# Kernel optimization log

Measured on AMD Instinct MI355X. Metric: run time of the kernel, lower is better.

Reference implementation:

```python
import jax, jax.numpy as jnp
import numpy as np


def setup_inputs() -> dict:
    key = jax.random.key(0)
    k0, k1, k2, k3, k4 = jax.random.split(key, 5)
    B, N, H, d, kproj = 4, 2048, 8, 32, 256
    queries = jax.random.normal(k0, (B, N, H, d), dtype=jnp.float32)
    keys = jax.random.normal(k1, (B, N, H, d), dtype=jnp.float32)
    values = jax.random.normal(k2, (B, N, H, d), dtype=jnp.float32)
    # Linformer sequence projections [N, k]; scaled so projected K/V keep unit-ish variance
    E_proj = jax.random.normal(k3, (N, kproj), dtype=jnp.float32) * 0.02
    F_proj = jax.random.normal(k4, (N, kproj), dtype=jnp.float32) * 0.02
    return {"queries": queries, "keys": keys, "values": values,
            "E_proj": E_proj, "F_proj": F_proj}


def reference(queries, keys, values, E_proj, F_proj):
    """Hybrid attention of dsfa_former:
      (1) FullAttention with triangular causal mask (manual einsum+softmax)
      (2) LinearAttentionHead: Linformer-style sequence projection of K/V via E/F.
    Dropout is identity (eval). Returns (out_full, out_lin), each [B, N, H, d].
    """
    B, N, H, d = queries.shape
    scale = 1.0 / jnp.sqrt(jnp.asarray(d, queries.dtype))

    # ---- FullAttention (causal) ----
    scores = jnp.einsum('blhe,bshe->bhls', queries, keys)  # [B,H,N,N]
    causal = jnp.triu(jnp.ones((N, N), dtype=bool), k=1)   # True above diag -> masked
    scores = jnp.where(causal, -jnp.inf, scores)
    A = jax.nn.softmax(scale * scores, axis=-1)
    out_full = jnp.einsum('bhls,bshd->blhd', A, values)    # [B,N,H,d]

    # ---- LinearAttentionHead (Linformer, no causal mask since kp != N) ----
    Qb = queries.transpose(0, 2, 1, 3)  # [B,H,N,d]
    Kb = keys.transpose(0, 2, 1, 3)
    Vb = values.transpose(0, 2, 1, 3)
    Kp = jnp.einsum('bhnd,nk->bhkd', Kb, E_proj)           # [B,H,k,d]
    Vp = jnp.einsum('bhnd,nk->bhkd', Vb, F_proj)           # [B,H,k,d]
    s_lin = jnp.einsum('bhnd,bhkd->bhnk', Qb, Kp) * scale  # d_k == d
    P = jax.nn.softmax(s_lin, axis=-1)
    out_lin = jnp.einsum('bhnk,bhkd->bhnd', P, Vp).transpose(0, 2, 1, 3)  # [B,N,H,d]

    return out_full, out_lin
```

## Files before the change

### kernel.cpp

```cpp
#include <hip/hip_runtime.h>
#include <hip/hip_bf16.h>


typedef __bf16 bf16x8 __attribute__((ext_vector_type(8)));
typedef __bf16 bf16x2 __attribute__((ext_vector_type(2)));
typedef float f32x4 __attribute__((ext_vector_type(4)));

union BF8 { uint4 u4; ushort us[8]; bf16x8 b; unsigned u32[4]; };

constexpr int B_ = 4, N_ = 2048, H_ = 8, D_ = 32, KP_ = 256, BH_ = 32;
constexpr float SCL2 = 0.25505654442633533f;
constexpr int NFULL = 1024;
constexpr int CHK = 32 * D_;

__device__ __forceinline__ ushort f2bf(float f) {
  unsigned u = __builtin_bit_cast(unsigned, f);
  return (ushort)((u + 0x7FFFu + ((u >> 16) & 1u)) >> 16);
}
__device__ __forceinline__ unsigned pkbf(float f0, float f1) {
#if __has_builtin(__builtin_amdgcn_cvt_pk_bf16_f32)
  bf16x2 r = __builtin_amdgcn_cvt_pk_bf16_f32(f0, f1);
  return __builtin_bit_cast(unsigned, r);
#else
  unsigned u0 = __builtin_bit_cast(unsigned, f0) + 0x8000u;
  unsigned u1 = __builtin_bit_cast(unsigned, f1) + 0x8000u;
  return __builtin_amdgcn_perm(u1, u0, 0x07060302);
#endif
}
__device__ __forceinline__ float bflo(unsigned u) {
  return __builtin_bit_cast(float, u << 16);
}
__device__ __forceinline__ float bfhi(unsigned u) {
  return __builtin_bit_cast(float, u & 0xFFFF0000u);
}
__device__ __forceinline__ float ex2(float x) {
#if __has_builtin(__builtin_amdgcn_exp2f)
  return __builtin_amdgcn_exp2f(x);
#else
  return exp2f(x);
#endif
}

__device__ __forceinline__ void load8_bf(const float* __restrict__ p,
                                         float scale, BF8& hi) {
  float4 a = *reinterpret_cast<const float4*>(p);
  float4 b = *reinterpret_cast<const float4*>(p + 4);
  float x[8] = {a.x, a.y, a.z, a.w, b.x, b.y, b.z, b.w};
#pragma unroll
  for (int i = 0; i < 8; ++i) hi.us[i] = f2bf(x[i] * scale);
}

__global__ __launch_bounds__(256) void k_prep(const float* __restrict__ K,
                                              const float* __restrict__ V,
                                              const float* __restrict__ E,
                                              const float* __restrict__ F,
                                              ushort* __restrict__ KH,
                                              ushort* __restrict__ Kt,
                                              ushort* __restrict__ Vt,
                                              ushort* __restrict__ Et,
                                              ushort* __restrict__ Ft) {
  __shared__ alignas(16) ushort S[4224];
  const int idx = blockIdx.x;
  const int t = threadIdx.x;
  if (idx < 1024) {
    ushort* Tk = S;
    ushort* Tv = S + 2112;
    const int bh = idx >> 5, b = bh >> 3, h = bh & 7;
    const int n0 = (idx & 31) * 64;
    {
      const int row = t >> 2, e8 = (t & 3) * 8;
      const size_t gbase = ((size_t)(b * N_ + n0 + row) * H_ + h) * D_ + e8;
      float4 k0 = *reinterpret_cast<const float4*>(K + gbase);
      float4 k1 = *reinterpret_cast<const float4*>(K + gbase + 4);
      float4 v0 = *reinterpret_cast<const float4*>(V + gbase);
      float4 v1 = *reinterpret_cast<const float4*>(V + gbase + 4);
      float kk[8] = {k0.x,k0.y,k0.z,k0.w,k1.x,k1.y,k1.z,k1.w};
      float vv[8] = {v0.x,v0.y,v0.z,v0.w,v1.x,v1.y,v1.z,v1.w};
      BF8 xh, vh;
#pragma unroll
      for (int i = 0; i < 4; ++i) {
        xh.u32[i] = pkbf(kk[2 * i], kk[2 * i + 1]);
        vh.u32[i] = pkbf(vv[2 * i], vv[2 * i + 1]);
      }
#pragma unroll
      for (int i = 0; i < 8; ++i) {
        Tk[(e8 + i) * 66 + row] = xh.us[i];
        Tv[(e8 + i) * 66 + row] = vh.us[i];
      }
      *reinterpret_cast<uint4*>(KH + ((size_t)bh * N_ + n0 + row) * D_ + e8) = xh.u4;
    }
    __syncthreads();
    {
      const int e = t >> 3, n8 = (t & 7) * 8;
      BF8 xk, xv;
#pragma unroll
      for (int i = 0; i < 8; ++i) {
        xk.us[i] = Tk[e * 66 + n8 + i];
        xv.us[i] = Tv[e * 66 + n8 + i];
      }
      const int c = (n0 + n8) >> 5, k = n8 & 31;
      const size_t ob = (((size_t)bh * 64 + c) * 32 + e) * 32 + k;
      *reinterpret_cast<uint4*>(Kt + ob) = xk.u4;
      *reinterpret_cast<uint4*>(Vt + ob) = xv.u4;
    }
  } else {
    const int j = idx - 1024;
    const float* src = (j >> 7) ? F : E;
    ushort* dst = (j >> 7) ? Ft : Et;
    const int jj = j & 127;
    const int n0 = (jj & 31) * 64, kp0 = (jj >> 5) * 64;
    ushort* T = S;
    {
      const int n = t >> 2, c16 = (t & 3) * 16;
      const size_t gbase = (size_t)(n0 + n) * KP_ + kp0 + c16;
#pragma unroll
      for (int q = 0; q < 4; ++q) {
        float4 x = *reinterpret_cast<const float4*>(src + gbase + q * 4);
        const unsigned u01 = pkbf(x.x, x.y), u23 = pkbf(x.z, x.w);
        T[(c16 + q * 4 + 0) * 66 + n] = (ushort)u01;
        T[(c16 + q * 4 + 1) * 66 + n] = (ushort)(u01 >> 16);
        T[(c16 + q * 4 + 2) * 66 + n] = (ushort)u23;
        T[(c16 + q * 4 + 3) * 66 + n] = (ushort)(u23 >> 16);
      }
    }
    __syncthreads();
    {
      const int kp = t >> 2, n16 = (t & 3) * 16;
      BF8 x0, x1;
#pragma unroll
      for (int i = 0; i < 8; ++i) {
        x0.us[i] = T[kp * 66 + n16 + i];
        x1.us[i] = T[kp * 66 + n16 + 8 + i];
      }
      const int c = (n0 + n16) >> 5, k = n16 & 31;
      const size_t ob = ((size_t)c * KP_ + kp0 + kp) * 32 + k;
      *reinterpret_cast<uint4*>(dst + ob) = x0.u4;
      *reinterpret_cast<uint4*>(dst + ob + 8) = x1.u4;
    }
  }
}

__global__ __launch_bounds__(512) void k_linproj(const ushort* __restrict__ Et,
                                                 const ushort* __restrict__ Ft,
                                                 const ushort* __restrict__ Kt,
                                                 const ushort* __restrict__ Vt,
                                                 ushort* __restrict__ Kp,
                                                 ushort* __restrict__ Vpt) {
  __shared__ float L[8][64][16];
  const int id = blockIdx.x;
  const int bh = (id & 7) + 8 * ((id >> 3) & 3);
  const int kp16 = (id >> 5) * 16;
  const int t = threadIdx.x;
  const int w = t >> 6, lane = t & 63, quad = lane >> 4, l15 = lane & 15;
  const int cbase = w * 8;

  const ushort* eA = Et + ((size_t)cbase * KP_ + kp16 + l15) * 32 + quad * 8;
  const ushort* fA = Ft + ((size_t)cbase * KP_ + kp16 + l15) * 32 + quad * 8;
  const ushort* kB0 = Kt + (((size_t)bh * 64 + cbase) * 32 + l15) * 32 + quad * 8;
  const ushort* kB1 = kB0 + 512;
  const ushort* vB0 = Vt + (((size_t)bh * 64 + cbase) * 32 + l15) * 32 + quad * 8;
  const ushort* vB1 = vB0 + 512;

  f32x4 accK0 = {0.f,0.f,0.f,0.f}, accK1 = {0.f,0.f,0.f,0.f};
  f32x4 accV0 = {0.f,0.f,0.f,0.f}, accV1 = {0.f,0.f,0.f,0.f};

  BF8 e0, f0, k00, k10, v00, v10;
  BF8 e1, f1, k01, k11, v01, v11;

#define LPLD(E, F, K0, K1, V0, V1, I)                                   \
  do {                                                                  \
    (E).u4 = *reinterpret_cast<const uint4*>(eA + (size_t)(I) * (KP_ * 32)); \
    (F).u4 = *reinterpret_cast<const uint4*>(fA + (size_t)(I) * (KP_ * 32)); \
    (K0).u4 = *reinterpret_cast<const uint4*>(kB0 + (I) * CHK);         \
    (K1).u4 = *reinterpret_cast<const uint4*>(kB1 + (I) * CHK);         \
    (V0).u4 = *reinterpret_cast<const uint4*>(vB0 + (I) * CHK);         \
    (V1).u4 = *reinterpret_cast<const uint4*>(vB1 + (I) * CHK);         \
  } while (0)
#define LPMM(E, F, K0, K1, V0, V1)                                            \
  do {                                                                        \
    accK0 = __builtin_amdgcn_mfma_f32_16x16x32_bf16((E).b, (K0).b, accK0, 0, 0, 0); \
    accK1 = __builtin_amdgcn_mfma_f32_16x16x32_bf16((E).b, (K1).b, accK1, 0, 0, 0); \
    accV0 = __builtin_amdgcn_mfma_f32_16x16x32_bf16((F).b, (V0).b, accV0, 0, 0, 0); \
    accV1 = __builtin_amdgcn_mfma_f32_16x16x32_bf16((F).b, (V1).b, accV1, 0, 0, 0); \
  } while (0)

  LPLD(e0, f0, k00, k10, v00, v10, 0);
  LPLD(e1, f1, k01, k11, v01, v11, 1);
#pragma unroll
  for (int p = 0; p < 3; ++p) {
    LPMM(e0, f0, k00, k10, v00, v10);
    LPLD(e0, f0, k00, k10, v00, v10, 2 * p + 2);
    LPMM(e1, f1, k01, k11, v01, v11);
    LPLD(e1, f1, k01, k11, v01, v11, 2 * p + 3);
  }
  LPMM(e0, f0, k00, k10, v00, v10);
  LPMM(e1, f1, k01, k11, v01, v11);
#undef LPLD
#undef LPMM

#pragma unroll
  for (int r = 0; r < 4; ++r) {
    L[w][lane][r]      = accK0[r];
    L[w][lane][4 + r]  = accK1[r];
    L[w][lane][8 + r]  = accV0[r];
    L[w][lane][12 + r] = accV1[r];
  }
  __syncthreads();
  if (w < 4) {
#pragma unroll
    for (int r = 0; r < 4; ++r) {
      const float v = ((L[0][lane][w * 4 + r] + L[1][lane][w * 4 + r]) +
                       (L[2][lane][w * 4 + r] + L[3][lane][w * 4 + r])) +
                      ((L[4][lane][w * 4 + r] + L[5][lane][w * 4 + r]) +
                       (L[6][lane][w * 4 + r] + L[7][lane][w * 4 + r]));
      const int kp = kp16 + quad * 4 + r;
      if (w == 0)      Kp[((size_t)bh * KP_ + kp) * D_ + l15]       = f2bf(v);
      else if (w == 1) Kp[((size_t)bh * KP_ + kp) * D_ + 16 + l15]  = f2bf(v);
      else if (w == 2)
        Vpt[(((size_t)bh * 8 + (kp >> 5)) * 32 + l15) * 32 + (kp & 31)] = f2bf(v);
      else
        Vpt[(((size_t)bh * 8 + (kp >> 5)) * 32 + 16 + l15) * 32 + (kp & 31)] = f2bf(v);
    }
  }
}

__global__ __launch_bounds__(256, 4) void k_attn(const float* __restrict__ Q,
                                                 const ushort* __restrict__ KH,
                                                 const ushort* __restrict__ Vt,
                                                 const ushort* __restrict__ Kp,
                                                 const ushort* __restrict__ Vpt,
                                                 float* __restrict__ out) {
  __shared__ alignas(16) unsigned Op[4][4][64][4];
  __shared__ float Ls[4][4][4][4];
  const int idx = blockIdx.x;
  const int t = threadIdx.x;
  const int w = t >> 6, lane = t & 63;
  const int quad = lane >> 4, l15 = lane & 15;
  const int kperm1 = 8 * (l15 >> 2) + (l15 & 3);
  const f32x4 z = {0.f,0.f,0.f,0.f};

  BF8 ones;
#pragma unroll
  for (int i2 = 0; i2 < 4; ++i2) ones.u32[i2] = 0x3F803F80u;

  const int bh = (idx & 7) + 8 * ((idx >> 3) & 3);
  const int m = 31 - (idx >> 5);
  const int b = bh >> 3, h = bh & 7;
  const int q0 = 64 * m;

  BF8 qh[4];
#pragma unroll
  for (int tt = 0; tt < 4; ++tt)
    load8_bf(Q + ((size_t)(b * N_ + q0 + 16 * tt + l15) * H_ + h) * D_ + quad * 8,
             SCL2, qh[tt]);

  {
    const ushort* KHl = KH + (size_t)bh * N_ * D_ + (size_t)kperm1 * D_ + quad * 8;
    const ushort* V0l = Vt + (size_t)bh * N_ * D_ + l15 * 32 + quad * 8;
    const ushort* V1l = V0l + 512;

    const int nun = 2 * m;
    const int cb = (w * nun) >> 2;
    const int ce = ((w + 1) * nun) >> 2;
    const int nwu = ce - cb;

    f32x4 O0[4], O1[4], LS[4];
#pragma unroll
    for (int tt = 0; tt < 4; ++tt) { O0[tt] = z; O1[tt] = z; LS[tt] = z; }

    BF8 kA1, kA2, vA0, vA1, kB1, kB2, vB0, vB1;

    auto procU = [&](BF8& k1, BF8& k2, BF8& v0, BF8& v1) {
      __builtin_amdgcn_s_setprio(1);
#pragma unroll
      for (int tt = 0; tt < 4; ++tt) {
        f32x4 s1 = __builtin_amdgcn_mfma_f32_16x16x32_bf16(k1.b, qh[tt].b, z, 0, 0, 0);
        f32x4 s2 = __builtin_amdgcn_mfma_f32_16x16x32_bf16(k2.b, qh[tt].b, z, 0, 0, 0);
        float e0 = ex2(s1[0]), e1 = ex2(s1[1]), e2 = ex2(s1[2]), e3 = ex2(s1[3]);
        float e4 = ex2(s2[0]), e5 = ex2(s2[1]), e6 = ex2(s2[2]), e7 = ex2(s2[3]);
        BF8 p;
        p.u32[0] = pkbf(e0, e1); p.u32[1] = pkbf(e2, e3);
        p.u32[2] = pkbf(e4, e5); p.u32[3] = pkbf(e6, e7);
        O0[tt] = __builtin_amdgcn_mfma_f32_16x16x32_bf16(p.b, v0.b, O0[tt], 0, 0, 0);
        O1[tt] = __builtin_amdgcn_mfma_f32_16x16x32_bf16(p.b, v1.b, O1[tt], 0, 0, 0);
        LS[tt] = __builtin_amdgcn_mfma_f32_16x16x32_bf16(p.b, ones.b, LS[tt], 0, 0, 0);
      }
      __builtin_amdgcn_s_setprio(0);
    };
    auto procM = [&](BF8& k1, BF8& k2, BF8& v0, BF8& v1, int ta, bool doUnm) {
      __builtin_amdgcn_s_setprio(1);
#pragma unroll
      for (int d = 0; d < 2; ++d) {
        const int tt = ta + d;
        const int thr = d ? 16 + l15 : l15;
        f32x4 s1 = __builtin_amdgcn_mfma_f32_16x16x32_bf16(k1.b, qh[tt].b, z, 0, 0, 0);
        f32x4 s2 = __builtin_amdgcn_mfma_f32_16x16x32_bf16(k2.b, qh[tt].b, z, 0, 0, 0);
        float e[8];
#pragma unroll
        for (int j = 0; j < 8; ++j) {
          const float sv = (j < 4) ? s1[j] : s2[j - 4];
          e[j] = (8 * quad + j <= thr) ? ex2(sv) : 0.f;
        }
        BF8 p;
        p.u32[0] = pkbf(e[0], e[1]); p.u32[1] = pkbf(e[2], e[3]);
        p.u32[2] = pkbf(e[4], e[5]); p.u32[3] = pkbf(e[6], e[7]);
        O0[tt] = __builtin_amdgcn_mfma_f32_16x16x32_bf16(p.b, v0.b, O0[tt], 0, 0, 0);
        O1[tt] = __builtin_amdgcn_mfma_f32_16x16x32_bf16(p.b, v1.b, O1[tt], 0, 0, 0);
        LS[tt] = __builtin_amdgcn_mfma_f32_16x16x32_bf16(p.b, ones.b, LS[tt], 0, 0, 0);
      }
      if (doUnm) {
#pragma unroll
        for (int tt = 2; tt < 4; ++tt) {
          f32x4 s1 = __builtin_amdgcn_mfma_f32_16x16x32_bf16(k1.b, qh[tt].b, z, 0, 0, 0);
          f32x4 s2 = __builtin_amdgcn_mfma_f32_16x16x32_bf16(k2.b, qh[tt].b, z, 0, 0, 0);
          float e0 = ex2(s1[0]), e1 = ex2(s1[1]), e2 = ex2(s1[2]), e3 = ex2(s1[3]);
          float e4 = ex2(s2[0]), e5 = ex2(s2[1]), e6 = ex2(s2[2]), e7 = ex2(s2[3]);
          BF8 p;
          p.u32[0] = pkbf(e0, e1); p.u32[1] = pkbf(e2, e3);
          p.u32[2] = pkbf(e4, e5); p.u32[3] = pkbf(e6, e7);
          O0[tt] = __builtin_amdgcn_mfma_f32_16x16x32_bf16(p.b, v0.b, O0[tt], 0, 0, 0);
          O1[tt] = __builtin_amdgcn_mfma_f32_16x16x32_bf16(p.b, v1.b, O1[tt], 0, 0, 0);
          LS[tt] = __builtin_amdgcn_mfma_f32_16x16x32_bf16(p.b, ones.b, LS[tt], 0, 0, 0);
        }
      }
      __builtin_amdgcn_s_setprio(0);
    };

    kA1.u4 = *reinterpret_cast<const uint4*>(KHl + (size_t)cb * CHK);
    kA2.u4 = *reinterpret_cast<const uint4*>(KHl + (size_t)cb * CHK + 4 * D_);
    vA0.u4 = *reinterpret_cast<const uint4*>(V0l + (size_t)cb * CHK);
    vA1.u4 = *reinterpret_cast<const uint4*>(V1l + (size_t)cb * CHK);
    kB1.u4 = *reinterpret_cast<const uint4*>(KHl + (size_t)(cb + 1) * CHK);
    kB2.u4 = *reinterpret_cast<const uint4*>(KHl + (size_t)(cb + 1) * CHK + 4 * D_);
    vB0.u4 = *reinterpret_cast<const uint4*>(V0l + (size_t)(cb + 1) * CHK);
    vB1.u4 = *reinterpret_cast<const uint4*>(V1l + (size_t)(cb + 1) * CHK);

    const ushort* pKA = KHl + (size_t)(cb + 2) * CHK;
    const ushort* pKB = KHl + (size_t)(cb + 3) * CHK;
    const ushort* pV0 = V0l + (size_t)(cb + 2) * CHK;
    const ushort* pV1 = V1l + (size_t)(cb + 2) * CHK;

    int i = 0;
    for (; i + 2 <= nwu; i += 2) {
      procU(kA1, kA2, vA0, vA1);
      kA1.u4 = *reinterpret_cast<const uint4*>(pKA);
      kA2.u4 = *reinterpret_cast<const uint4*>(pKA + 4 * D_);
      vA0.u4 = *reinterpret_cast<const uint4*>(pV0);
      vA1.u4 = *reinterpret_cast<const uint4*>(pV1);
      procU(kB1, kB2, vB0, vB1);
      kB1.u4 = *reinterpret_cast<const uint4*>(pKB);
      kB2.u4 = *reinterpret_cast<const uint4*>(pKB + 4 * D_);
      vB0.u4 = *reinterpret_cast<const uint4*>(pV0 + CHK);
      vB1.u4 = *reinterpret_cast<const uint4*>(pV1 + CHK);
      pKA += 2 * CHK; pKB += 2 * CHK; pV0 += 2 * CHK; pV1 += 2 * CHK;
    }
    if (i < nwu) {
      procU(kA1, kA2, vA0, vA1);
      if (w == 3) procM(kB1, kB2, vB0, vB1, 0, true);
    } else if (w == 3) {
      procM(kA1, kA2, vA0, vA1, 0, true);
    }
    if (w == 2) {
      const int c2 = nun + 1;
      kB1.u4 = *reinterpret_cast<const uint4*>(KHl + (size_t)c2 * CHK);
      kB2.u4 = *reinterpret_cast<const uint4*>(KHl + (size_t)c2 * CHK + 4 * D_);
      vB0.u4 = *reinterpret_cast<const uint4*>(V0l + (size_t)c2 * CHK);
      vB1.u4 = *reinterpret_cast<const uint4*>(V1l + (size_t)c2 * CHK);
      procM(kB1, kB2, vB0, vB1, 2, false);
    }

#pragma unroll
    for (int tt = 0; tt < 4; ++tt) {
      uint4 pk;
      pk.x = pkbf(O0[tt][0], O0[tt][1]);
      pk.y = pkbf(O0[tt][2], O0[tt][3]);
      pk.z = pkbf(O1[tt][0], O1[tt][1]);
      pk.w = pkbf(O1[tt][2], O1[tt][3]);
      *reinterpret_cast<uint4*>(Op[w][tt][lane]) = pk;
    }
    if (l15 == 0) {
#pragma unroll
      for (int tt = 0; tt < 4; ++tt)
#pragma unroll
        for (int r = 0; r < 4; ++r) Ls[w][tt][quad][r] = LS[tt][r];
    }
    __syncthreads();
    {
      const int tt = w;
      float iv[4];
#pragma unroll
      for (int r = 0; r < 4; ++r) {
        const float l = Ls[0][tt][quad][r] + Ls[1][tt][quad][r] +
                        Ls[2][tt][quad][r] + Ls[3][tt][quad][r];
        iv[r] = __builtin_amdgcn_rcpf(l);
      }
      float A0[4] = {0.f,0.f,0.f,0.f}, A1[4] = {0.f,0.f,0.f,0.f};
#pragma unroll
      for (int s = 0; s < 4; ++s) {
        const uint4 u = *reinterpret_cast<const uint4*>(Op[s][tt][lane]);
        A0[0] += bflo(u.x); A0[1] += bfhi(u.x);
        A0[2] += bflo(u.y); A0[3] += bfhi(u.y);
        A1[0] += bflo(u.z); A1[1] += bfhi(u.z);
        A1[2] += bflo(u.w); A1[3] += bfhi(u.w);
      }
#pragma unroll
      for (int r = 0; r < 4; ++r) {
        const int q = q0 + 16 * tt + quad * 4 + r;
        const size_t base = ((size_t)(b * N_ + q) * H_ + h) * D_;
        out[base + l15]      = A0[r] * iv[r];
        out[base + 16 + l15] = A1[r] * iv[r];
      }
    }
  }

  {
    BF8 qsel = qh[0];
    if (w == 1) qsel = qh[1];
    else if (w == 2) qsel = qh[2];
    else if (w == 3) qsel = qh[3];

    float* olin = out + (size_t)B_ * N_ * H_ * D_;
    const int q0l = q0 + 16 * w;

    const int kperm2 = kperm1 + 4;
    const ushort* KpHb = Kp + (size_t)bh * KP_ * D_ + quad * 8;
    const ushort* Vp0 = Vpt + (size_t)bh * KP_ * D_ + l15 * 32 + quad * 8;
    const ushort* Vp1 = Vp0 + 512;

    f32x4 LSum = z, O0 = z, O1 = z;
    __builtin_amdgcn_s_setprio(1);
#pragma unroll
    for (int g = 0; g < 8; ++g) {
      const int kp0 = g * 32;
      BF8 a1, a2, v0, v1;
      a1.u4 = *reinterpret_cast<const uint4*>(KpHb + (size_t)(kp0 + kperm1) * D_);
      a2.u4 = *reinterpret_cast<const uint4*>(KpHb + (size_t)(kp0 + kperm2) * D_);
      v0.u4 = *reinterpret_cast<const uint4*>(Vp0 + g * CHK);
      v1.u4 = *reinterpret_cast<const uint4*>(Vp1 + g * CHK);
      f32x4 s1 = __builtin_amdgcn_mfma_f32_16x16x32_bf16(a1.b, qsel.b, z, 0, 0, 0);
      f32x4 s2 = __builtin_amdgcn_mfma_f32_16x16x32_bf16(a2.b, qsel.b, z, 0, 0, 0);
      const float e0 = ex2(s1[0]), e1 = ex2(s1[1]), e2 = ex2(s1[2]), e3 = ex2(s1[3]);
      const float e4 = ex2(s2[0]), e5 = ex2(s2[1]), e6 = ex2(s2[2]), e7 = ex2(s2[3]);
      BF8 p;
      p.u32[0] = pkbf(e0, e1); p.u32[1] = pkbf(e2, e3);
      p.u32[2] = pkbf(e4, e5); p.u32[3] = pkbf(e6, e7);
      LSum = __builtin_amdgcn_mfma_f32_16x16x32_bf16(p.b, ones.b, LSum, 0, 0, 0);
      O0 = __builtin_amdgcn_mfma_f32_16x16x32_bf16(p.b, v0.b, O0, 0, 0, 0);
      O1 = __builtin_amdgcn_mfma_f32_16x16x32_bf16(p.b, v1.b, O1, 0, 0, 0);
    }
    __builtin_amdgcn_s_setprio(0);

#pragma unroll
    for (int r = 0; r < 4; ++r) {
      const float fr = __builtin_amdgcn_rcpf(LSum[r]);
      const int q = q0l + quad * 4 + r;
      const size_t base = ((size_t)(b * N_ + q) * H_ + h) * D_;
      olin[base + l15]      = O0[r] * fr;
      olin[base + 16 + l15] = O1[r] * fr;
    }
  }
}

extern "C" void kernel_launch(void* const* d_in, const int* in_sizes, int n_in,
                              void* d_out, int out_size, void* d_ws, size_t ws_size,
                              hipStream_t stream) {
  const float* Q = (const float*)d_in[0];
  const float* K = (const float*)d_in[1];
  const float* V = (const float*)d_in[2];
  const float* E = (const float*)d_in[3];
  const float* F = (const float*)d_in[4];
  float* out = (float*)d_out;

  ushort* KH  = (ushort*)d_ws;
  ushort* Kt  = KH + (size_t)BH_ * N_ * D_;
  ushort* Vt  = Kt + (size_t)BH_ * N_ * D_;
  ushort* Et  = Vt + (size_t)BH_ * N_ * D_;
  ushort* Ft  = Et + (size_t)KP_ * N_;
  ushort* Kp  = Ft + (size_t)KP_ * N_;
  ushort* Vpt = Kp + (size_t)BH_ * KP_ * D_;

  k_prep<<<dim3(1280), 256, 0, stream>>>(K, V, E, F, KH, Kt, Vt, Et, Ft);
  k_linproj<<<dim3(512), 512, 0, stream>>>(Et, Ft, Kt, Vt, Kp, Vpt);
  k_attn<<<dim3(NFULL), 256, 0, stream>>>(Q, KH, Vt, Kp, Vpt, out);
}
```

Baseline: 122.6 us.

## Pre-convert Q to bf16 in prep and store K/Kp in MFMA-fragment layout

Q is now scaled and converted to bf16 in the prep kernel and written in a per-tile fragment layout, so the attention kernel loads ready-made bf16 operands instead of fp32 with per-element conversion. KH and Kp are likewise stored in a lane-permuted chunk layout, so each lane's MFMA operand is a contiguous 16-byte read at laneoff instead of a strided row gather. This cuts global traffic and conversion work in k_attn at the cost of an extra bf16 Q write and more workspace in the prep stage.

```diff
diff --git a/kernel.cpp b/kernel.cpp
--- a/kernel.cpp
+++ b/kernel.cpp
@@ -41,16 +41,8 @@
 #endif
 }
 
-__device__ __forceinline__ void load8_bf(const float* __restrict__ p,
-                                         float scale, BF8& hi) {
-  float4 a = *reinterpret_cast<const float4*>(p);
-  float4 b = *reinterpret_cast<const float4*>(p + 4);
-  float x[8] = {a.x, a.y, a.z, a.w, b.x, b.y, b.z, b.w};
-#pragma unroll
-  for (int i = 0; i < 8; ++i) hi.us[i] = f2bf(x[i] * scale);
-}
-
-__global__ __launch_bounds__(256) void k_prep(const float* __restrict__ K,
+__global__ __launch_bounds__(256) void k_prep(const float* __restrict__ Qf,
+                                              const float* __restrict__ K,
                                               const float* __restrict__ V,
                                               const float* __restrict__ E,
                                               const float* __restrict__ F,
@@ -58,7 +50,8 @@
                                               ushort* __restrict__ Kt,
                                               ushort* __restrict__ Vt,
                                               ushort* __restrict__ Et,
-                                              ushort* __restrict__ Ft) {
+                                              ushort* __restrict__ Ft,
+                                              ushort* __restrict__ QH) {
   __shared__ alignas(16) ushort S[4224];
   const int idx = blockIdx.x;
   const int t = threadIdx.x;
@@ -74,20 +67,37 @@
       float4 k1 = *reinterpret_cast<const float4*>(K + gbase + 4);
       float4 v0 = *reinterpret_cast<const float4*>(V + gbase);
       float4 v1 = *reinterpret_cast<const float4*>(V + gbase + 4);
+      float4 q0 = *reinterpret_cast<const float4*>(Qf + gbase);
+      float4 q1 = *reinterpret_cast<const float4*>(Qf + gbase + 4);
       float kk[8] = {k0.x,k0.y,k0.z,k0.w,k1.x,k1.y,k1.z,k1.w};
       float vv[8] = {v0.x,v0.y,v0.z,v0.w,v1.x,v1.y,v1.z,v1.w};
-      BF8 xh, vh;
+      float qq[8] = {q0.x,q0.y,q0.z,q0.w,q1.x,q1.y,q1.z,q1.w};
+      BF8 xh, vh, qp;
 #pragma unroll
       for (int i = 0; i < 4; ++i) {
         xh.u32[i] = pkbf(kk[2 * i], kk[2 * i + 1]);
         vh.u32[i] = pkbf(vv[2 * i], vv[2 * i + 1]);
+        qp.u32[i] = pkbf(qq[2 * i] * SCL2, qq[2 * i + 1] * SCL2);
       }
 #pragma unroll
       for (int i = 0; i < 8; ++i) {
         Tk[(e8 + i) * 66 + row] = xh.us[i];
         Tv[(e8 + i) * 66 + row] = vh.us[i];
       }
-      *reinterpret_cast<uint4*>(KH + ((size_t)bh * N_ + n0 + row) * D_ + e8) = xh.u4;
+      {
+        const int n32 = row & 31;
+        const int cg = (idx & 31) * 2 + (row >> 5);
+        const int half = (n32 >> 2) & 1;
+        const int l15p = 4 * (n32 >> 3) + (n32 & 3);
+        *reinterpret_cast<uint4*>(
+            KH + (((size_t)bh * 64 + cg) * 2 + half) * 512 + l15p * 32 + e8) = xh.u4;
+      }
+      {
+        const int mq = idx & 31;
+        const int tq = (row >> 4) & 3, l15q = row & 15;
+        *reinterpret_cast<uint4*>(
+            QH + (((size_t)bh * 32 + mq) * 4 + tq) * 512 + l15q * 32 + e8) = qp.u4;
+      }
     }
     __syncthreads();
     {
@@ -214,17 +224,22 @@
                       ((L[4][lane][w * 4 + r] + L[5][lane][w * 4 + r]) +
                        (L[6][lane][w * 4 + r] + L[7][lane][w * 4 + r]));
       const int kp = kp16 + quad * 4 + r;
-      if (w == 0)      Kp[((size_t)bh * KP_ + kp) * D_ + l15]       = f2bf(v);
-      else if (w == 1) Kp[((size_t)bh * KP_ + kp) * D_ + 16 + l15]  = f2bf(v);
-      else if (w == 2)
+      if (w < 2) {
+        const int g = kp >> 5, n32 = kp & 31;
+        const int half = (n32 >> 2) & 1;
+        const int l15p = 4 * (n32 >> 3) + (n32 & 3);
+        const int e = (w == 0) ? l15 : 16 + l15;
+        Kp[(((size_t)bh * 8 + g) * 2 + half) * 512 + l15p * 32 + e] = f2bf(v);
+      } else if (w == 2) {
         Vpt[(((size_t)bh * 8 + (kp >> 5)) * 32 + l15) * 32 + (kp & 31)] = f2bf(v);
-      else
+      } else {
         Vpt[(((size_t)bh * 8 + (kp >> 5)) * 32 + 16 + l15) * 32 + (kp & 31)] = f2bf(v);
-    }
-  }
-}
-
-__global__ __launch_bounds__(256, 4) void k_attn(const float* __restrict__ Q,
+      }
+    }
+  }
+}
+
+__global__ __launch_bounds__(256, 4) void k_attn(const ushort* __restrict__ QH,
                                                  const ushort* __restrict__ KH,
                                                  const ushort* __restrict__ Vt,
                                                  const ushort* __restrict__ Kp,
@@ -236,7 +251,6 @@
   const int t = threadIdx.x;
   const int w = t >> 6, lane = t & 63;
   const int quad = lane >> 4, l15 = lane & 15;
-  const int kperm1 = 8 * (l15 >> 2) + (l15 & 3);
   const f32x4 z = {0.f,0.f,0.f,0.f};
 
   BF8 ones;
@@ -247,15 +261,18 @@
   const int m = 31 - (idx >> 5);
   const int b = bh >> 3, h = bh & 7;
   const int q0 = 64 * m;
+  const int laneoff = l15 * 32 + quad * 8;
 
   BF8 qh[4];
-#pragma unroll
-  for (int tt = 0; tt < 4; ++tt)
-    load8_bf(Q + ((size_t)(b * N_ + q0 + 16 * tt + l15) * H_ + h) * D_ + quad * 8,
-             SCL2, qh[tt]);
-
   {
-    const ushort* KHl = KH + (size_t)bh * N_ * D_ + (size_t)kperm1 * D_ + quad * 8;
+    const ushort* QHl = QH + (((size_t)bh * 32 + m) * 4) * 512 + laneoff;
+#pragma unroll
+    for (int tt = 0; tt < 4; ++tt)
+      qh[tt].u4 = *reinterpret_cast<const uint4*>(QHl + tt * 512);
+  }
+
+  {
+    const ushort* KHl = KH + (size_t)bh * N_ * D_ + laneoff;
     const ushort* V0l = Vt + (size_t)bh * N_ * D_ + l15 * 32 + quad * 8;
     const ushort* V1l = V0l + 512;
 
@@ -327,11 +344,11 @@
     };
 
     kA1.u4 = *reinterpret_cast<const uint4*>(KHl + (size_t)cb * CHK);
-    kA2.u4 = *reinterpret_cast<const uint4*>(KHl + (size_t)cb * CHK + 4 * D_);
+    kA2.u4 = *reinterpret_cast<const uint4*>(KHl + (size_t)cb * CHK + 512);
     vA0.u4 = *reinterpret_cast<const uint4*>(V0l + (size_t)cb * CHK);
     vA1.u4 = *reinterpret_cast<const uint4*>(V1l + (size_t)cb * CHK);
     kB1.u4 = *reinterpret_cast<const uint4*>(KHl + (size_t)(cb + 1) * CHK);
-    kB2.u4 = *reinterpret_cast<const uint4*>(KHl + (size_t)(cb + 1) * CHK + 4 * D_);
+    kB2.u4 = *reinterpret_cast<const uint4*>(KHl + (size_t)(cb + 1) * CHK + 512);
     vB0.u4 = *reinterpret_cast<const uint4*>(V0l + (size_t)(cb + 1) * CHK);
     vB1.u4 = *reinterpret_cast<const uint4*>(V1l + (size_t)(cb + 1) * CHK);
 
@@ -344,12 +361,12 @@
     for (; i + 2 <= nwu; i += 2) {
       procU(kA1, kA2, vA0, vA1);
       kA1.u4 = *reinterpret_cast<const uint4*>(pKA);
-      kA2.u4 = *reinterpret_cast<const uint4*>(pKA + 4 * D_);
+      kA2.u4 = *reinterpret_cast<const uint4*>(pKA + 512);
       vA0.u4 = *reinterpret_cast<const uint4*>(pV0);
       vA1.u4 = *reinterpret_cast<const uint4*>(pV1);
       procU(kB1, kB2, vB0, vB1);
       kB1.u4 = *reinterpret_cast<const uint4*>(pKB);
-      kB2.u4 = *reinterpret_cast<const uint4*>(pKB + 4 * D_);
+      kB2.u4 = *reinterpret_cast<const uint4*>(pKB + 512);
       vB0.u4 = *reinterpret_cast<const uint4*>(pV0 + CHK);
       vB1.u4 = *reinterpret_cast<const uint4*>(pV1 + CHK);
       pKA += 2 * CHK; pKB += 2 * CHK; pV0 += 2 * CHK; pV1 += 2 * CHK;
@@ -363,7 +380,7 @@
     if (w == 2) {
       const int c2 = nun + 1;
       kB1.u4 = *reinterpret_cast<const uint4*>(KHl + (size_t)c2 * CHK);
-      kB2.u4 = *reinterpret_cast<const uint4*>(KHl + (size_t)c2 * CHK + 4 * D_);
+      kB2.u4 = *reinterpret_cast<const uint4*>(KHl + (size_t)c2 * CHK + 512);
       vB0.u4 = *reinterpret_cast<const uint4*>(V0l + (size_t)c2 * CHK);
       vB1.u4 = *reinterpret_cast<const uint4*>(V1l + (size_t)c2 * CHK);
       procM(kB1, kB2, vB0, vB1, 2, false);
@@ -422,8 +439,7 @@
     float* olin = out + (size_t)B_ * N_ * H_ * D_;
     const int q0l = q0 + 16 * w;
 
-    const int kperm2 = kperm1 + 4;
-    const ushort* KpHb = Kp + (size_t)bh * KP_ * D_ + quad * 8;
+    const ushort* KpL = Kp + (size_t)bh * KP_ * D_ + laneoff;
     const ushort* Vp0 = Vpt + (size_t)bh * KP_ * D_ + l15 * 32 + quad * 8;
     const ushort* Vp1 = Vp0 + 512;
 
@@ -431,10 +447,9 @@
     __builtin_amdgcn_s_setprio(1);
 #pragma unroll
     for (int g = 0; g < 8; ++g) {
-      const int kp0 = g * 32;
       BF8 a1, a2, v0, v1;
-      a1.u4 = *reinterpret_cast<const uint4*>(KpHb + (size_t)(kp0 + kperm1) * D_);
-      a2.u4 = *reinterpret_cast<const uint4*>(KpHb + (size_t)(kp0 + kperm2) * D_);
+      a1.u4 = *reinterpret_cast<const uint4*>(KpL + g * CHK);
+      a2.u4 = *reinterpret_cast<const uint4*>(KpL + g * CHK + 512);
       v0.u4 = *reinterpret_cast<const uint4*>(Vp0 + g * CHK);
       v1.u4 = *reinterpret_cast<const uint4*>(Vp1 + g * CHK);
       f32x4 s1 = __builtin_amdgcn_mfma_f32_16x16x32_bf16(a1.b, qsel.b, z, 0, 0, 0);
@@ -478,8 +493,9 @@
   ushort* Ft  = Et + (size_t)KP_ * N_;
   ushort* Kp  = Ft + (size_t)KP_ * N_;
   ushort* Vpt = Kp + (size_t)BH_ * KP_ * D_;
-
-  k_prep<<<dim3(1280), 256, 0, stream>>>(K, V, E, F, KH, Kt, Vt, Et, Ft);
+  ushort* QHP = Vpt + (size_t)BH_ * KP_ * D_;
+
+  k_prep<<<dim3(1280), 256, 0, stream>>>(Q, K, V, E, F, KH, Kt, Vt, Et, Ft, QHP);
   k_linproj<<<dim3(512), 512, 0, stream>>>(Et, Ft, Kt, Vt, Kp, Vpt);
-  k_attn<<<dim3(NFULL), 256, 0, stream>>>(Q, KH, Vt, Kp, Vpt, out);
-}
+  k_attn<<<dim3(NFULL), 256, 0, stream>>>(QHP, KH, Vt, Kp, Vpt, out);
+}
```

Result: no change. 122.5 us (-0.1%).
